# Kernel tuning notes

Hardware: AMD Instinct MI355X
Metric: run time of the kernel (lower is better)

The kernel has to match this reference:

```python
import jax, jax.numpy as jnp
import numpy as np

S = 0.1          # slab half-width: |sum(y)| <= S
R2 = 0.02        # ball radius squared: ||y||^2 <= R2
EPS = 1e-12


def _project(z):
    """Euclidean projection of each row of z onto {y : |1^T y|<=S, ||y||^2<=R2}.

    KKT case analysis:
      1) project onto slab only; accept if inside ball
      2) project onto ball only; accept if inside slab
      3) both constraints active: y = c*z + ((sign(t)*S - c*t)/n)*1 with
         c = sqrt((n*R2 - S^2) / (n*||z||^2 - t^2)),  t = 1^T z.
    """
    n = z.shape[-1]
    t = jnp.sum(z, axis=-1, keepdims=True)                       # [B,1]
    zz = jnp.sum(z * z, axis=-1, keepdims=True)                  # [B,1]

    # case 1: slab projection (contains z itself when already feasible)
    y1 = z + (jnp.clip(t, -S, S) - t) / n
    ok1 = jnp.sum(y1 * y1, axis=-1, keepdims=True) <= R2

    # case 2: ball projection
    znorm = jnp.sqrt(jnp.maximum(zz, EPS))
    scale = jnp.minimum(1.0, jnp.sqrt(R2) / znorm)
    y2 = z * scale
    ok2 = jnp.abs(t) * scale <= S

    # case 3: both active
    denom = jnp.maximum(n * zz - t * t, EPS)                     # >= 0 by Cauchy-Schwarz
    c = jnp.sqrt(jnp.maximum(n * R2 - S * S, 0.0) / denom)
    sp = jnp.sign(t) * S
    y3 = c * z + (sp - c * t) / n

    return jnp.where(ok1, y1, jnp.where(ok2, y2, y3))


def setup_inputs() -> dict:
    key = jax.random.key(0)
    k1, k2, k3 = jax.random.split(key, 3)
    B, D_in, D_out = 65536, 512, 256
    x = jax.random.normal(k1, (B, D_in), dtype=jnp.float32)
    # params (scaled so z = W@x - b straddles the feasible region boundary)
    W = 0.01 * jax.random.normal(k2, (D_out, D_in), dtype=jnp.float32)
    b = 0.01 * jax.random.normal(k3, (D_out,), dtype=jnp.float32)
    return {"x": x, "W": W, "b": b}


def reference(x, W, b):
    z = x @ W.T - b                                              # [B, D_out]
    return _project(z)
```

## Files before the change

kernel.cpp:

```cpp
#include <hip/hip_runtime.h>


typedef __bf16 bf16x8 __attribute__((ext_vector_type(8)));
typedef float f32x4 __attribute__((ext_vector_type(4)));

#define BM 128
#define BN 256
#define BK 64
#define LDA 72
#define THREADS 512

__device__ __forceinline__ unsigned short f2bf(float f) {
    unsigned u = __builtin_bit_cast(unsigned, f);
    u += 0x7fffu + ((u >> 16) & 1u);
    return (unsigned short)(u >> 16);
}

__global__ void wconv_kernel(const float* __restrict__ W,
                             unsigned short* __restrict__ Wb) {
    int i = (blockIdx.x * 256 + threadIdx.x) * 4;
    float4 v = *(const float4*)(W + i);
    ushort4 h;
    h.x = f2bf(v.x); h.y = f2bf(v.y); h.z = f2bf(v.z); h.w = f2bf(v.w);
    *(ushort4*)(Wb + i) = h;
}

__global__ __launch_bounds__(THREADS, 4)
void proj_gemm_kernel(const float* __restrict__ x,
                      const unsigned short* __restrict__ Wb,
                      const float* __restrict__ b,
                      float* __restrict__ out) {
    __shared__ alignas(16) unsigned short Abuf[BM * LDA];
    __shared__ alignas(16) unsigned short Bbuf[BN * BK];

    const int tid  = threadIdx.x;
    const int lane = tid & 63;
    const int wv   = tid >> 6;
    const int wm   = wv >> 2;
    const int wn   = wv & 3;
    const int ln   = lane & 15;
    const int quad = lane >> 4;
    const int m0   = blockIdx.x * BM;

    const int arow = tid >> 4;
    const int kq   = tid & 15;
    const float* xbase = x + (long)(m0 + arow) * 512 + kq * 4;

    const int b_r0 = wv * 32 + (lane >> 3);
    const int b_cg = (lane & 7) ^ (lane >> 3);

    f32x4 acc[4][4];
    #pragma unroll
    for (int mi = 0; mi < 4; ++mi)
        #pragma unroll
        for (int ni = 0; ni < 4; ++ni)
            acc[mi][ni] = (f32x4){0.f, 0.f, 0.f, 0.f};

    for (int kt = 0; kt < 8; ++kt) {
        const int k0 = kt * BK;
        __syncthreads();
        #pragma unroll
        for (int j = 0; j < 4; ++j) {
            const unsigned short* src =
                Wb + (long)(b_r0 + j * 8) * 512 + k0 + b_cg * 8;
            __builtin_amdgcn_global_load_lds(
                (const __attribute__((address_space(1))) void*)src,
                (__attribute__((address_space(3))) void*)(unsigned long)(unsigned int)
                    (unsigned long)(uintptr_t)&Bbuf[(wv * 4 + j) * 512],
                16, 0, 0);
        }
        #pragma unroll
        for (int p = 0; p < 4; ++p) {
            const int row = arow + p * 32;
            float4 v = *(const float4*)(xbase + (long)p * 32 * 512 + k0);
            ushort4 h;
            h.x = f2bf(v.x); h.y = f2bf(v.y); h.z = f2bf(v.z); h.w = f2bf(v.w);
            *(ushort4*)&Abuf[row * LDA + kq * 4] = h;
        }
        __syncthreads();
        #pragma unroll
        for (int ks = 0; ks < 2; ++ks) {
            bf16x8 bf[4];
            #pragma unroll
            for (int ni = 0; ni < 4; ++ni) {
                const int r  = wn * 64 + ni * 16 + ln;
                const int cc = (ks * 4 + quad) ^ (ln & 7);
                bf[ni] = *(const bf16x8*)&Bbuf[r * 64 + cc * 8];
            }
            #pragma unroll
            for (int mi = 0; mi < 4; ++mi) {
                const int row = wm * 64 + mi * 16 + ln;
                bf16x8 af = *(const bf16x8*)&Abuf[row * LDA + ks * 32 + quad * 8];
                #pragma unroll
                for (int ni = 0; ni < 4; ++ni)
                    acc[mi][ni] = __builtin_amdgcn_mfma_f32_16x16x32_bf16(
                        af, bf[ni], acc[mi][ni], 0, 0, 0);
            }
        }
    }

    float bb[4];
    #pragma unroll
    for (int ni = 0; ni < 4; ++ni) bb[ni] = b[wn * 64 + ni * 16 + ln];
    #pragma unroll
    for (int mi = 0; mi < 4; ++mi)
        #pragma unroll
        for (int ni = 0; ni < 4; ++ni)
            #pragma unroll
            for (int r = 0; r < 4; ++r)
                acc[mi][ni][r] -= bb[ni];

    __syncthreads();
    float* P  = (float*)Abuf;
    float* AB = P + 128 * 8;

    #pragma unroll
    for (int mi = 0; mi < 4; ++mi) {
        #pragma unroll
        for (int r = 0; r < 4; ++r) {
            float s1 = 0.f, s2 = 0.f;
            #pragma unroll
            for (int ni = 0; ni < 4; ++ni) {
                float v = acc[mi][ni][r];
                s1 += v; s2 += v * v;
            }
            #pragma unroll
            for (int off = 1; off < 16; off <<= 1) {
                s1 += __shfl_xor(s1, off, 64);
                s2 += __shfl_xor(s2, off, 64);
            }
            if (ln == 0) {
                int row = wm * 64 + mi * 16 + quad * 4 + r;
                P[row * 8 + wn * 2 + 0] = s1;
                P[row * 8 + wn * 2 + 1] = s2;
            }
        }
    }
    __syncthreads();

    if (tid < 128) {
        int row = tid;
        float t  = P[row*8+0] + P[row*8+2] + P[row*8+4] + P[row*8+6];
        float zz = P[row*8+1] + P[row*8+3] + P[row*8+5] + P[row*8+7];
        const float S = 0.1f, R2 = 0.02f, nf = 256.f, inv_n = 1.f / 256.f;
        float tc    = fminf(fmaxf(t, -S), S);
        float beta1 = (tc - t) * inv_n;
        float ny1   = zz + 2.f * beta1 * t + nf * beta1 * beta1;
        float alpha, beta;
        if (ny1 <= R2) {
            alpha = 1.f; beta = beta1;
        } else {
            float znorm = sqrtf(fmaxf(zz, 1e-12f));
            float scale = fminf(1.f, 0.14142135623730951f / znorm);
            if (fabsf(t) * scale <= S) {
                alpha = scale; beta = 0.f;
            } else {
                float denom = fmaxf(nf * zz - t * t, 1e-12f);
                float c  = sqrtf(5.11f / denom);
                float sp = (t > 0.f) ? S : ((t < 0.f) ? -S : 0.f);
                alpha = c; beta = (sp - c * t) * inv_n;
            }
        }
        AB[row*2+0] = alpha;
        AB[row*2+1] = beta;
    }
    __syncthreads();

    #pragma unroll
    for (int mi = 0; mi < 4; ++mi) {
        #pragma unroll
        for (int r = 0; r < 4; ++r) {
            int row = wm * 64 + mi * 16 + quad * 4 + r;
            float alpha = AB[row*2+0];
            float beta  = AB[row*2+1];
            float* orow = out + (long)(m0 + row) * 256 + wn * 64 + ln;
            #pragma unroll
            for (int ni = 0; ni < 4; ++ni)
                orow[ni*16] = alpha * acc[mi][ni][r] + beta;
        }
    }
}

extern "C" void kernel_launch(void* const* d_in, const int* in_sizes, int n_in,
                              void* d_out, int out_size, void* d_ws, size_t ws_size,
                              hipStream_t stream) {
    const float* x = (const float*)d_in[0];
    const float* W = (const float*)d_in[1];
    const float* b = (const float*)d_in[2];
    float* out = (float*)d_out;
    unsigned short* Wb = (unsigned short*)d_ws;

    const int Dout = in_sizes[2];
    const int Din  = in_sizes[1] / Dout;
    const int Btot = in_sizes[0] / Din;

    wconv_kernel<<<(Dout * Din) / (256 * 4), 256, 0, stream>>>(W, Wb);
    proj_gemm_kernel<<<Btot / BM, THREADS, 0, stream>>>(x, Wb, b, out);
}
```

Measured before the change: 219.9 us.

## Drop LDS staging and load GEMM operands directly from global into registers

The GEMM kernel no longer stages x and W tiles through shared memory with block-wide barriers. Each wave now loads its fp32 x fragments and bf16 W fragments straight from global memory in MFMA operand layout and converts x to bf16 in registers. The block shrinks to 64 rows and 4 waves, each covering all 64 rows and a 64-column slice. This removes LDS traffic and the barriers in the K loop, but each wave now re-reads the x rows and W is fetched redundantly across many blocks, so the design depends on L1/L2 cache hits. The row-stride access pattern may also coalesce less well.

```diff
diff --git a/kernel.cpp b/kernel.cpp
--- a/kernel.cpp
+++ b/kernel.cpp
@@ -4,11 +4,8 @@
 typedef __bf16 bf16x8 __attribute__((ext_vector_type(8)));
 typedef float f32x4 __attribute__((ext_vector_type(4)));
 
-#define BM 128
-#define BN 256
-#define BK 64
-#define LDA 72
-#define THREADS 512
+#define THREADS 256
+#define BM 64
 
 __device__ __forceinline__ unsigned short f2bf(float f) {
     unsigned u = __builtin_bit_cast(unsigned, f);
@@ -25,29 +22,36 @@
     *(ushort4*)(Wb + i) = h;
 }
 
-__global__ __launch_bounds__(THREADS, 4)
+__device__ __forceinline__ bf16x8 cvt8(float4 a, float4 b) {
+    bf16x8 r;
+    r[0] = (__bf16)a.x; r[1] = (__bf16)a.y; r[2] = (__bf16)a.z; r[3] = (__bf16)a.w;
+    r[4] = (__bf16)b.x; r[5] = (__bf16)b.y; r[6] = (__bf16)b.z; r[7] = (__bf16)b.w;
+    return r;
+}
+
+__global__ __launch_bounds__(THREADS, 3)
 void proj_gemm_kernel(const float* __restrict__ x,
                       const unsigned short* __restrict__ Wb,
-                      const float* __restrict__ b,
+                      const float* __restrict__ bias,
                       float* __restrict__ out) {
-    __shared__ alignas(16) unsigned short Abuf[BM * LDA];
-    __shared__ alignas(16) unsigned short Bbuf[BN * BK];
+    __shared__ float P[BM * 8];
+    __shared__ float AB[BM * 2];
 
     const int tid  = threadIdx.x;
     const int lane = tid & 63;
-    const int wv   = tid >> 6;
-    const int wm   = wv >> 2;
-    const int wn   = wv & 3;
+    const int wn   = tid >> 6;
     const int ln   = lane & 15;
     const int quad = lane >> 4;
-    const int m0   = blockIdx.x * BM;
+    const long m0  = (long)blockIdx.x * BM;
 
-    const int arow = tid >> 4;
-    const int kq   = tid & 15;
-    const float* xbase = x + (long)(m0 + arow) * 512 + kq * 4;
-
-    const int b_r0 = wv * 32 + (lane >> 3);
-    const int b_cg = (lane & 7) ^ (lane >> 3);
+    const float* xa[4];
+    #pragma unroll
+    for (int mi = 0; mi < 4; ++mi)
+        xa[mi] = x + (m0 + mi * 16 + ln) * 512 + quad * 8;
+    const unsigned short* wb[4];
+    #pragma unroll
+    for (int ni = 0; ni < 4; ++ni)
+        wb[ni] = Wb + (long)(wn * 64 + ni * 16 + ln) * 512 + quad * 8;
 
     f32x4 acc[4][4];
     #pragma unroll
@@ -56,52 +60,32 @@
         for (int ni = 0; ni < 4; ++ni)
             acc[mi][ni] = (f32x4){0.f, 0.f, 0.f, 0.f};
 
-    for (int kt = 0; kt < 8; ++kt) {
-        const int k0 = kt * BK;
-        __syncthreads();
+    #pragma unroll 2
+    for (int k = 0; k < 16; ++k) {
+        const int k0 = k * 32;
+        float4 a0[4], a1[4];
         #pragma unroll
-        for (int j = 0; j < 4; ++j) {
-            const unsigned short* src =
-                Wb + (long)(b_r0 + j * 8) * 512 + k0 + b_cg * 8;
-            __builtin_amdgcn_global_load_lds(
-                (const __attribute__((address_space(1))) void*)src,
-                (__attribute__((address_space(3))) void*)(unsigned long)(unsigned int)
-                    (unsigned long)(uintptr_t)&Bbuf[(wv * 4 + j) * 512],
-                16, 0, 0);
+        for (int mi = 0; mi < 4; ++mi) {
+            a0[mi] = *(const float4*)(xa[mi] + k0);
+            a1[mi] = *(const float4*)(xa[mi] + k0 + 4);
         }
+        bf16x8 bf[4];
         #pragma unroll
-        for (int p = 0; p < 4; ++p) {
-            const int row = arow + p * 32;
-            float4 v = *(const float4*)(xbase + (long)p * 32 * 512 + k0);
-            ushort4 h;
-            h.x = f2bf(v.x); h.y = f2bf(v.y); h.z = f2bf(v.z); h.w = f2bf(v.w);
-            *(ushort4*)&Abuf[row * LDA + kq * 4] = h;
-        }
-        __syncthreads();
+        for (int ni = 0; ni < 4; ++ni)
+            bf[ni] = *(const bf16x8*)(wb[ni] + k0);
         #pragma unroll
-        for (int ks = 0; ks < 2; ++ks) {
-            bf16x8 bf[4];
+        for (int mi = 0; mi < 4; ++mi) {
+            bf16x8 af = cvt8(a0[mi], a1[mi]);
             #pragma unroll
-            for (int ni = 0; ni < 4; ++ni) {
-                const int r  = wn * 64 + ni * 16 + ln;
-                const int cc = (ks * 4 + quad) ^ (ln & 7);
-                bf[ni] = *(const bf16x8*)&Bbuf[r * 64 + cc * 8];
-            }
-            #pragma unroll
-            for (int mi = 0; mi < 4; ++mi) {
-                const int row = wm * 64 + mi * 16 + ln;
-                bf16x8 af = *(const bf16x8*)&Abuf[row * LDA + ks * 32 + quad * 8];
-                #pragma unroll
-                for (int ni = 0; ni < 4; ++ni)
-                    acc[mi][ni] = __builtin_amdgcn_mfma_f32_16x16x32_bf16(
-                        af, bf[ni], acc[mi][ni], 0, 0, 0);
-            }
+            for (int ni = 0; ni < 4; ++ni)
+                acc[mi][ni] = __builtin_amdgcn_mfma_f32_16x16x32_bf16(
+                    af, bf[ni], acc[mi][ni], 0, 0, 0);
         }
     }
 
     float bb[4];
     #pragma unroll
-    for (int ni = 0; ni < 4; ++ni) bb[ni] = b[wn * 64 + ni * 16 + ln];
+    for (int ni = 0; ni < 4; ++ni) bb[ni] = bias[wn * 64 + ni * 16 + ln];
     #pragma unroll
     for (int mi = 0; mi < 4; ++mi)
         #pragma unroll
@@ -109,10 +93,6 @@
             #pragma unroll
             for (int r = 0; r < 4; ++r)
                 acc[mi][ni][r] -= bb[ni];
-
-    __syncthreads();
-    float* P  = (float*)Abuf;
-    float* AB = P + 128 * 8;
 
     #pragma unroll
     for (int mi = 0; mi < 4; ++mi) {
@@ -130,7 +110,7 @@
                 s2 += __shfl_xor(s2, off, 64);
             }
             if (ln == 0) {
-                int row = wm * 64 + mi * 16 + quad * 4 + r;
+                int row = mi * 16 + quad * 4 + r;
                 P[row * 8 + wn * 2 + 0] = s1;
                 P[row * 8 + wn * 2 + 1] = s2;
             }
@@ -138,7 +118,7 @@
     }
     __syncthreads();
 
-    if (tid < 128) {
+    if (tid < BM) {
         int row = tid;
         float t  = P[row*8+0] + P[row*8+2] + P[row*8+4] + P[row*8+6];
         float zz = P[row*8+1] + P[row*8+3] + P[row*8+5] + P[row*8+7];
@@ -170,10 +150,10 @@
     for (int mi = 0; mi < 4; ++mi) {
         #pragma unroll
         for (int r = 0; r < 4; ++r) {
-            int row = wm * 64 + mi * 16 + quad * 4 + r;
+            int row = mi * 16 + quad * 4 + r;
             float alpha = AB[row*2+0];
             float beta  = AB[row*2+1];
-            float* orow = out + (long)(m0 + row) * 256 + wn * 64 + ln;
+            float* orow = out + (m0 + row) * 256 + wn * 64 + ln;
             #pragma unroll
             for (int ni = 0; ni < 4; ++ni)
                 orow[ni*16] = alpha * acc[mi][ni][r] + beta;
```

Measured after the change: 275.5 us. 25.3% more time.
